# Kernel tuning notes

Hardware: AMD Instinct MI355X
Metric: run time of the kernel (lower is better)

Reference implementation:

```python
import jax, jax.numpy as jnp
import numpy as np

N_HEADS = 8   # n_heads
L = 2         # num_layers (= args.upper_T_num_layers)
H = 64        # hidden_size (= args.upper_T_hidden_dim)
F = 64        # input features
T = 12        # seq_len (= args.n_his)
N = 16384     # node_num (= LSTM batch dim)


def setup_inputs() -> dict:
    key = jax.random.key(0)
    ks = jax.random.split(key, 10)
    s = 0.05
    x = jax.random.normal(ks[0], (T, N, F), jnp.float32)
    # Stacked per-head, per-layer LSTM weights (PyTorch gate order: i, f, g, o).
    # Layer 0 input dim F == H so all layers stack cleanly.
    W_ih = jax.random.normal(ks[1], (L, N_HEADS, 4 * H, H), jnp.float32) * s
    W_hh = jax.random.normal(ks[2], (L, N_HEADS, 4 * H, H), jnp.float32) * s
    b_ih = jax.random.normal(ks[3], (L, N_HEADS, 4 * H), jnp.float32) * s
    b_hh = jax.random.normal(ks[4], (L, N_HEADS, 4 * H), jnp.float32) * s
    # Learned initial states (xavier-init nn.Parameters in the original).
    h0 = jax.random.normal(ks[5], (N_HEADS, L, N, H), jnp.float32) * s
    c0 = jax.random.normal(ks[6], (N_HEADS, L, N, H), jnp.float32) * s
    # 1x1 Conv2d(n_heads*n_his -> n_his): pure channel mixing.
    conv_w = jax.random.normal(ks[7], (T, N_HEADS * T), jnp.float32) * s
    conv_b = jax.random.normal(ks[8], (T,), jnp.float32) * s
    return {"x": x, "W_ih": W_ih, "W_hh": W_hh, "b_ih": b_ih, "b_hh": b_hh,
            "h0": h0, "c0": c0, "conv_w": conv_w, "conv_b": conv_b}


def _scan_lstm(gi, Whh, bhh, h0, c0):
    # gi: (T, heads, N, 4H) precomputed input contribution; h0/c0: (heads, N, H)
    def step(carry, g_t):
        h, c = carry
        gates = g_t + jnp.einsum('and,agd->ang', h, Whh) + bhh[:, None, :]
        i, f, g, o = jnp.split(gates, 4, axis=-1)
        c = jax.nn.sigmoid(f) * c + jax.nn.sigmoid(i) * jnp.tanh(g)
        h = jax.nn.sigmoid(o) * jnp.tanh(c)
        return (h, c), h
    (_, _), hs = jax.lax.scan(step, (h0, c0), gi)
    return hs  # (T, heads, N, H)


def reference(x, W_ih, W_hh, b_ih, b_hh, h0, c0, conv_w, conv_b):
    n_layers, n_heads = W_ih.shape[0], W_ih.shape[1]
    t_len, n_nodes, _ = x.shape
    hdim = W_hh.shape[-1]
    # Layer 0: input x is shared across heads; precompute input gates outside scan.
    gi = jnp.einsum('tnd,agd->tang', x, W_ih[0]) + b_ih[0][None, :, None, :]
    hs = _scan_lstm(gi, W_hh[0], b_hh[0], h0[:, 0], c0[:, 0])
    for l in range(1, n_layers):
        gi = jnp.einsum('tand,agd->tang', hs, W_ih[l]) + b_ih[l][None, :, None, :]
        hs = _scan_lstm(gi, W_hh[l], b_hh[l], h0[:, l], c0[:, l])
    # torch.cat over heads: head-major, then time -> channel dim = heads*T
    cat = jnp.transpose(hs, (1, 0, 2, 3)).reshape(n_heads * t_len, n_nodes, hdim)
    # 1x1 conv == channel mixing over (heads*T) -> T
    out = jnp.einsum('cnh,oc->onh', cat, conv_w) + conv_b[:, None, None]
    return out[None]  # (1, T, N, H)
```

## Files before the change

### kernel.cpp

```cpp
#include <hip/hip_runtime.h>
#include <hip/hip_bf16.h>


#define T_LEN 12
#define NHEADS 8
#define HD 64
#define NNODES 16384
#define MT 16
#define LDSP 72
#define WIH_ELEMS (2 * NHEADS * 4 * HD * HD)

typedef __bf16 bf16_t;
typedef __attribute__((ext_vector_type(2))) __bf16 bf16x2;
typedef __attribute__((ext_vector_type(4))) __bf16 bf16x4;
typedef __attribute__((ext_vector_type(8))) __bf16 bf16x8;
typedef __attribute__((ext_vector_type(4))) float f32x4;

#define MFMA16(a, b, c) __builtin_amdgcn_mfma_f32_16x16x32_bf16((a), (b), (c), 0, 0, 0)

#if __has_builtin(__builtin_amdgcn_exp2f)
#define EXP2(x) __builtin_amdgcn_exp2f(x)
#else
#define EXP2(x) exp2f(x)
#endif

__device__ __forceinline__ float fast_sigmoid(float v) {
    return __builtin_amdgcn_rcpf(1.0f + __expf(-v));
}
__device__ __forceinline__ float fast_tanh(float v) {
    return 2.0f * __builtin_amdgcn_rcpf(1.0f + __expf(-2.0f * v)) - 1.0f;
}

__device__ __forceinline__ bf16x8 load8f(const float* p) {
    f32x4 a = *(const f32x4*)p;
    f32x4 b = *(const f32x4*)(p + 4);
    bf16x8 r;
    r[0] = (bf16_t)a[0]; r[1] = (bf16_t)a[1]; r[2] = (bf16_t)a[2]; r[3] = (bf16_t)a[3];
    r[4] = (bf16_t)b[0]; r[5] = (bf16_t)b[1]; r[6] = (bf16_t)b[2]; r[7] = (bf16_t)b[3];
    return r;
}
__device__ __forceinline__ bf16x4 load4f(const float* p) {
    f32x4 a = *(const f32x4*)p;
    bf16x4 r;
    r[0] = (bf16_t)a[0]; r[1] = (bf16_t)a[1]; r[2] = (bf16_t)a[2]; r[3] = (bf16_t)a[3];
    return r;
}

template<bool SC>
__device__ __forceinline__ bf16x4 lstm_pointwise_sw(const f32x4* acc, float* creg) {
    float cn[4], so[4], tc[4];
    #pragma unroll
    for (int r = 0; r < 4; ++r) {
        float ei, ef, eg, eo;
        if (SC) {
            ei = EXP2(-acc[0][r]); ef = EXP2(-acc[1][r]);
            eg = EXP2(-acc[2][r]); eo = EXP2(-acc[3][r]);
        } else {
            ei = __expf(-acc[0][r]); ef = __expf(-acc[1][r]);
            eg = __expf(-2.0f * acc[2][r]); eo = __expf(-acc[3][r]);
        }
        float di = 1.0f + ei, df = 1.0f + ef, dg = 1.0f + eg, do_ = 1.0f + eo;
        float pif = di * df, pgo = dg * do_;
        float rr  = __builtin_amdgcn_rcpf(pif * pgo);
        float rif = rr * pgo, rgo = rr * pif;
        float sig_i  = rif * df;
        float sig_f  = rif * di;
        float tanh_g = 2.0f * (rgo * do_) - 1.0f;
        so[r] = rgo * dg;
        float cnr = sig_f * creg[r] + sig_i * tanh_g;
        cn[r] = cnr;
        creg[r] = cnr;
    }
    float d0 = 1.0f + EXP2(cn[0] * -2.885390082f);
    float d1 = 1.0f + EXP2(cn[1] * -2.885390082f);
    float d2 = 1.0f + EXP2(cn[2] * -2.885390082f);
    float d3 = 1.0f + EXP2(cn[3] * -2.885390082f);
    float p01 = d0 * d1, p23 = d2 * d3;
    float rr  = __builtin_amdgcn_rcpf(p01 * p23);
    float r01 = rr * p23, r23 = rr * p01;
    tc[0] = 2.0f * (r01 * d1) - 1.0f;
    tc[1] = 2.0f * (r01 * d0) - 1.0f;
    tc[2] = 2.0f * (r23 * d3) - 1.0f;
    tc[3] = 2.0f * (r23 * d2) - 1.0f;
    bf16x4 hv;
    hv[0] = (bf16_t)(so[0] * tc[0]);
    hv[1] = (bf16_t)(so[1] * tc[1]);
    hv[2] = (bf16_t)(so[2] * tc[2]);
    hv[3] = (bf16_t)(so[3] * tc[3]);
    return hv;
}

__global__ __launch_bounds__(256) void cvt_bf16_kernel(
    const float* __restrict__ src, bf16_t* __restrict__ dst, int n8)
{
    int i = blockIdx.x * 256 + threadIdx.x;
    if (i < n8) *(bf16x8*)(dst + (size_t)i * 8) = load8f(src + (size_t)i * 8);
}

__global__ __launch_bounds__(256) void cvt_w_kernel(
    const float* __restrict__ src, bf16_t* __restrict__ dst, int n8)
{
    int i = blockIdx.x * 256 + threadIdx.x;
    if (i >= n8) return;
    int row  = (i >> 3) & 255;
    int gate = row >> 6;
    float sc = (gate == 2) ? 2.885390082f : 1.442695041f;
    const float* p = src + (size_t)i * 8;
    f32x4 a = *(const f32x4*)p;
    f32x4 b = *(const f32x4*)(p + 4);
    bf16x8 r;
    r[0] = (bf16_t)(a[0]*sc); r[1] = (bf16_t)(a[1]*sc);
    r[2] = (bf16_t)(a[2]*sc); r[3] = (bf16_t)(a[3]*sc);
    r[4] = (bf16_t)(b[0]*sc); r[5] = (bf16_t)(b[1]*sc);
    r[6] = (bf16_t)(b[2]*sc); r[7] = (bf16_t)(b[3]*sc);
    *(bf16x8*)(dst + (size_t)i * 8) = r;
}

template<bool PREP>
__global__ __launch_bounds__(512, 4) void lstm_pipe_kernel(
    const float* __restrict__ xg,
    const bf16_t* __restrict__ xbf,
    const float* __restrict__ Wih,
    const float* __restrict__ Whh,
    const bf16_t* __restrict__ wbf,
    const float* __restrict__ bih,
    const float* __restrict__ bhh,
    const float* __restrict__ h0g,
    const float* __restrict__ c0g,
    bf16_t* __restrict__ hsw)
{
    __shared__ __align__(16) bf16_t xT[T_LEN][MT][LDSP];
    __shared__ __align__(16) bf16_t h0A[2][MT][LDSP];
    __shared__ __align__(16) bf16_t h1H[T_LEN + 1][MT][LDSP];
    __shared__ __align__(16) float  biasLds[2][4][4][16];

    const int tid  = threadIdx.x;
    const int w    = tid >> 6;
    const int lane = tid & 63;
    const int quad = lane >> 4;
    const int col  = lane & 15;
    const int lw   = w >> 2;
    const int wq   = w & 3;
    const int a    = blockIdx.x & (NHEADS - 1);
    const int nb   = (blockIdx.x >> 3) * MT;

    #pragma unroll
    for (int it = 0; it < 3; ++it) {
        int e    = (it * 512 + tid) * 8;
        int t    = e >> 10;
        int node = (e >> 6) & (MT - 1);
        int f    = e & (HD - 1);
        bf16x8 v;
        if (PREP) v = *(const bf16x8*)(xbf + ((size_t)t * NNODES + nb + node) * HD + f);
        else      v = load8f(xg + ((size_t)t * NNODES + nb + node) * HD + f);
        *(bf16x8*)&xT[t][node][f] = v;
    }
    {
        int e    = tid * 4;
        int l    = e >> 10;
        int node = (e >> 6) & (MT - 1);
        int hh   = e & (HD - 1);
        bf16x4 v = load4f(h0g + (((size_t)a * 2 + l) * NNODES + nb + node) * HD + hh);
        if (l == 0) *(bf16x4*)&h0A[0][node][hh] = v;
        else        *(bf16x4*)&h1H[0][node][hh] = v;
    }
    {
        int l   = tid >> 8;
        int r   = tid & 255;
        int wqi = r >> 6;
        int nii = (r >> 4) & 3;
        int gc  = r & 15;
        int off = (l * NHEADS + a) * 256 + nii * 64 + wqi * 16 + gc;
        float sc = PREP ? (nii == 2 ? 2.885390082f : 1.442695041f) : 1.0f;
        biasLds[l][wqi][nii][gc] = (bih[off] + bhh[off]) * sc;
    }

    bf16x8 wA[4][2], wB[4][2];
    #pragma unroll
    for (int ni = 0; ni < 4; ++ni)
        #pragma unroll
        for (int kf = 0; kf < 2; ++kf) {
            size_t off = (((size_t)lw * NHEADS + a) * 256 + (4 * ni + wq) * 16 + col) * HD
                       + kf * 32 + quad * 8;
            if (PREP) {
                wA[ni][kf] = *(const bf16x8*)(wbf + off);
                wB[ni][kf] = *(const bf16x8*)(wbf + WIH_ELEMS + off);
            } else {
                wA[ni][kf] = load8f(Wih + off);
                wB[ni][kf] = load8f(Whh + off);
            }
        }
    float creg[4];
    {
        f32x4 cv = *(const f32x4*)(c0g + (((size_t)a * 2 + lw) * NNODES + nb + col) * HD
                                   + wq * 16 + quad * 4);
        creg[0] = cv[0]; creg[1] = cv[1]; creg[2] = cv[2]; creg[3] = cv[3];
    }
    __syncthreads();

    int cur = 0;
    #pragma unroll 1
    for (int p = 0; p <= T_LEN; ++p) {
        const bool active = lw ? (p >= 1) : (p < T_LEN);
        if (active) {
            const bf16_t* P = lw ? &h0A[cur][0][0]     : &xT[p][0][0];
            const bf16_t* Q = lw ? &h1H[p - 1][0][0]   : &h0A[cur][0][0];
            bf16_t*       D = lw ? &h1H[p][0][0]       : &h0A[cur ^ 1][0][0];
            const int ro = col * LDSP + quad * 8;
            bf16x8 a0 = *(const bf16x8*)(P + ro);
            bf16x8 b0 = *(const bf16x8*)(Q + ro);
            f32x4 acc[4];
            #pragma unroll
            for (int ni = 0; ni < 4; ++ni) {
                f32x4 z = *(const f32x4*)&biasLds[lw][wq][ni][quad * 4];
                z = MFMA16(wA[ni][0], a0, z);
                acc[ni] = MFMA16(wB[ni][0], b0, z);
            }
            bf16x8 a1 = *(const bf16x8*)(P + ro + 32);
            bf16x8 b1 = *(const bf16x8*)(Q + ro + 32);
            #pragma unroll
            for (int ni = 0; ni < 4; ++ni) {
                f32x4 z = MFMA16(wA[ni][1], a1, acc[ni]);
                acc[ni] = MFMA16(wB[ni][1], b1, z);
            }
            bf16x4 hv = lstm_pointwise_sw<PREP>(acc, creg);
            *(bf16x4*)(D + col * LDSP + wq * 16 + quad * 4) = hv;
        }
        __syncthreads();
        cur ^= 1;
    }

    #pragma unroll
    for (int it = 0; it < 3; ++it) {
        int i    = it * 512 + tid;
        int t    = i >> 7;
        int c    = i & 127;
        int node = c >> 3;
        int h8   = (c & 7) * 8;
        *(bf16x8*)(hsw + ((size_t)(a * T_LEN + t) * NNODES + nb + node) * HD + h8) =
            *(const bf16x8*)&h1H[t + 1][node][h8];
    }
}

__global__ __launch_bounds__(256) void conv_reduce_kernel(
    const bf16_t* __restrict__ hsw,
    const float* __restrict__ cwg,
    const float* __restrict__ cbg,
    float* __restrict__ outg)
{
    int flat = blockIdx.x * 256 + threadIdx.x;
    int n  = flat >> 4;
    int h4 = (flat & 15) * 4;
    f32x4 acc[T_LEN];
    #pragma unroll
    for (int o = 0; o < T_LEN; ++o) {
        float b = cbg[o];
        acc[o][0] = b; acc[o][1] = b; acc[o][2] = b; acc[o][3] = b;
    }
    const bf16_t* src = hsw + (size_t)n * HD + h4;
    #pragma unroll 6
    for (int c = 0; c < NHEADS * T_LEN; ++c) {
        bf16x4 hv = *(const bf16x4*)(src + (size_t)c * NNODES * HD);
        float h0 = (float)hv[0], h1 = (float)hv[1], h2 = (float)hv[2], h3 = (float)hv[3];
        #pragma unroll
        for (int o = 0; o < T_LEN; ++o) {
            float cv = cwg[o * (NHEADS * T_LEN) + c];
            acc[o][0] += cv * h0; acc[o][1] += cv * h1;
            acc[o][2] += cv * h2; acc[o][3] += cv * h3;
        }
    }
    #pragma unroll
    for (int o = 0; o < T_LEN; ++o)
        *(f32x4*)(outg + ((size_t)o * NNODES + n) * HD + h4) = acc[o];
}

struct SmemT {
    __align__(16) bf16_t xT[T_LEN][MT][LDSP];
    __align__(16) bf16_t hA[2][2][MT][LDSP];
    __align__(16) float  cwf[T_LEN][NHEADS * T_LEN];
    __align__(16) float  cbf[T_LEN];
};

__global__ __launch_bounds__(256) void lstm_mono_kernel(
    const float* __restrict__ xg, const float* __restrict__ Wih,
    const float* __restrict__ Whh, const float* __restrict__ bih,
    const float* __restrict__ bhh, const float* __restrict__ h0g,
    const float* __restrict__ c0g, const float* __restrict__ cwg,
    const float* __restrict__ cbg, float* __restrict__ outg)
{
    __shared__ SmemT s;
    const int tid  = threadIdx.x;
    const int w    = tid >> 6;
    const int lane = tid & 63;
    const int quad = lane >> 4;
    const int col  = lane & 15;
    const int nb   = blockIdx.x * MT;

    #pragma unroll
    for (int it = 0; it < 6; ++it) {
        int ci   = it * 256 + tid;
        int e    = ci * 8;
        int t    = e >> 10;
        int node = (e >> 6) & (MT - 1);
        int f    = e & (HD - 1);
        *(bf16x8*)&s.xT[t][node][f] =
            load8f(xg + ((size_t)t * NNODES + nb + node) * HD + f);
    }
    for (int i = tid; i < T_LEN * NHEADS * T_LEN; i += 256)
        s.cwf[i / 96][i % 96] = cwg[i];
    if (tid < T_LEN) s.cbf[tid] = cbg[tid];

    float conv_acc[T_LEN][4];
    #pragma unroll
    for (int o = 0; o < T_LEN; ++o)
        #pragma unroll
        for (int r = 0; r < 4; ++r) conv_acc[o][r] = 0.0f;

    #pragma unroll 1
    for (int a = 0; a < NHEADS; ++a) {
        bf16x8 wih[2][4][2], whh[2][4][2];
        #pragma unroll
        for (int l = 0; l < 2; ++l)
            #pragma unroll
            for (int ni = 0; ni < 4; ++ni)
                #pragma unroll
                for (int kf = 0; kf < 2; ++kf) {
                    size_t off = (((size_t)l * NHEADS + a) * 256 + (4 * ni + w) * 16 + col) * HD
                               + kf * 32 + quad * 8;
                    wih[l][ni][kf] = load8f(Wih + off);
                    whh[l][ni][kf] = load8f(Whh + off);
                }
        float bias[2][4];
        #pragma unroll
        for (int l = 0; l < 2; ++l)
            #pragma unroll
            for (int ni = 0; ni < 4; ++ni) {
                int off = (l * NHEADS + a) * 256 + ni * 64 + w * 16 + col;
                bias[l][ni] = bih[off] + bhh[off];
            }
        float creg[2][4];
        #pragma unroll
        for (int l = 0; l < 2; ++l)
            #pragma unroll
            for (int r = 0; r < 4; ++r)
                creg[l][r] = c0g[(((size_t)a * 2 + l) * NNODES + nb + quad * 4 + r) * HD
                                 + w * 16 + col];
        {
            int e    = tid * 8;
            int l    = e >> 10;
            int node = (e >> 6) & (MT - 1);
            int hh   = e & (HD - 1);
            *(bf16x8*)&s.hA[l][0][node][hh] =
                load8f(h0g + (((size_t)a * 2 + l) * NNODES + nb + node) * HD + hh);
        }
        __syncthreads();

        int cur = 0;
        #pragma unroll 1
        for (int t = 0; t < T_LEN; ++t) {
            bf16x8 xa0 = *(const bf16x8*)&s.xT[t][col][quad * 8];
            bf16x8 xa1 = *(const bf16x8*)&s.xT[t][col][32 + quad * 8];
            bf16x8 ha0 = *(const bf16x8*)&s.hA[0][cur][col][quad * 8];
            bf16x8 ha1 = *(const bf16x8*)&s.hA[0][cur][col][32 + quad * 8];
            f32x4 acc[4];
            #pragma unroll
            for (int ni = 0; ni < 4; ++ni) {
                f32x4 z = {0.f, 0.f, 0.f, 0.f};
                z = MFMA16(xa0, wih[0][ni][0], z);
                z = MFMA16(xa1, wih[0][ni][1], z);
                z = MFMA16(ha0, whh[0][ni][0], z);
                z = MFMA16(ha1, whh[0][ni][1], z);
                acc[ni] = z;
            }
            #pragma unroll
            for (int r = 0; r < 4; ++r) {
                float ig = fast_sigmoid(acc[0][r] + bias[0][0]);
                float fg = fast_sigmoid(acc[1][r] + bias[0][1]);
                float gg = fast_tanh   (acc[2][r] + bias[0][2]);
                float og = fast_sigmoid(acc[3][r] + bias[0][3]);
                float cn = fg * creg[0][r] + ig * gg;
                creg[0][r] = cn;
                s.hA[0][cur ^ 1][quad * 4 + r][w * 16 + col] = (bf16_t)(og * fast_tanh(cn));
            }
            __syncthreads();
            bf16x8 pa0 = *(const bf16x8*)&s.hA[0][cur ^ 1][col][quad * 8];
            bf16x8 pa1 = *(const bf16x8*)&s.hA[0][cur ^ 1][col][32 + quad * 8];
            bf16x8 qa0 = *(const bf16x8*)&s.hA[1][cur][col][quad * 8];
            bf16x8 qa1 = *(const bf16x8*)&s.hA[1][cur][col][32 + quad * 8];
            #pragma unroll
            for (int ni = 0; ni < 4; ++ni) {
                f32x4 z = {0.f, 0.f, 0.f, 0.f};
                z = MFMA16(pa0, wih[1][ni][0], z);
                z = MFMA16(pa1, wih[1][ni][1], z);
                z = MFMA16(qa0, whh[1][ni][0], z);
                z = MFMA16(qa1, whh[1][ni][1], z);
                acc[ni] = z;
            }
            float hn[4];
            #pragma unroll
            for (int r = 0; r < 4; ++r) {
                float ig = fast_sigmoid(acc[0][r] + bias[1][0]);
                float fg = fast_sigmoid(acc[1][r] + bias[1][1]);
                float gg = fast_tanh   (acc[2][r] + bias[1][2]);
                float og = fast_sigmoid(acc[3][r] + bias[1][3]);
                float cn = fg * creg[1][r] + ig * gg;
                creg[1][r] = cn;
                hn[r] = og * fast_tanh(cn);
                s.hA[1][cur ^ 1][quad * 4 + r][w * 16 + col] = (bf16_t)hn[r];
            }
            #pragma unroll
            for (int o = 0; o < T_LEN; ++o) {
                float cv = s.cwf[o][a * T_LEN + t];
                #pragma unroll
                for (int r = 0; r < 4; ++r) conv_acc[o][r] += cv * hn[r];
            }
            __syncthreads();
            cur ^= 1;
        }
    }
    #pragma unroll
    for (int o = 0; o < T_LEN; ++o)
        #pragma unroll
        for (int r = 0; r < 4; ++r)
            outg[((size_t)o * NNODES + nb + quad * 4 + r) * HD + w * 16 + col] =
                conv_acc[o][r] + s.cbf[o];
}

extern "C" void kernel_launch(void* const* d_in, const int* in_sizes, int n_in,
                              void* d_out, int out_size, void* d_ws, size_t ws_size,
                              hipStream_t stream) {
    (void)in_sizes; (void)n_in; (void)out_size;
    const float* x   = (const float*)d_in[0];
    const float* Wih = (const float*)d_in[1];
    const float* Whh = (const float*)d_in[2];
    const float* bih = (const float*)d_in[3];
    const float* bhh = (const float*)d_in[4];
    const float* h0  = (const float*)d_in[5];
    const float* c0  = (const float*)d_in[6];
    const float* cw  = (const float*)d_in[7];
    const float* cb  = (const float*)d_in[8];
    const size_t hs_bytes = (size_t)NHEADS * T_LEN * NNODES * HD * sizeof(bf16_t);
    const size_t x_bytes  = (size_t)T_LEN * NNODES * HD * sizeof(bf16_t);
    const size_t w_bytes  = (size_t)2 * WIH_ELEMS * sizeof(bf16_t);
    if (ws_size >= hs_bytes + x_bytes + w_bytes) {
        bf16_t* hs  = (bf16_t*)d_ws;
        bf16_t* xbf = (bf16_t*)((char*)d_ws + hs_bytes);
        bf16_t* wbf = (bf16_t*)((char*)d_ws + hs_bytes + x_bytes);
        const int n8x = T_LEN * NNODES * HD / 8;
        const int n8w = WIH_ELEMS / 8;
        cvt_bf16_kernel<<<dim3(n8x / 256), dim3(256), 0, stream>>>(x, xbf, n8x);
        cvt_w_kernel<<<dim3((n8w + 255) / 256), dim3(256), 0, stream>>>(Wih, wbf, n8w);
        cvt_w_kernel<<<dim3((n8w + 255) / 256), dim3(256), 0, stream>>>(Whh, wbf + WIH_ELEMS, n8w);
        lstm_pipe_kernel<true><<<dim3((NNODES / MT) * NHEADS), dim3(512), 0, stream>>>(
            x, xbf, Wih, Whh, wbf, bih, bhh, h0, c0, hs);
        conv_reduce_kernel<<<dim3(NNODES * 16 / 256), dim3(256), 0, stream>>>(
            hs, cw, cb, (float*)d_out);
    } else if (ws_size >= hs_bytes) {
        bf16_t* hs = (bf16_t*)d_ws;
        lstm_pipe_kernel<false><<<dim3((NNODES / MT) * NHEADS), dim3(512), 0, stream>>>(
            x, nullptr, Wih, Whh, nullptr, bih, bhh, h0, c0, hs);
        conv_reduce_kernel<<<dim3(NNODES * 16 / 256), dim3(256), 0, stream>>>(
            hs, cw, cb, (float*)d_out);
    } else {
        lstm_mono_kernel<<<dim3(NNODES / MT), dim3(256), 0, stream>>>(
            x, Wih, Whh, bih, bhh, h0, c0, cw, cb, (float*)d_out);
    }
}
```

Before: 514.8 us.

## Store hidden states node-major, split per-layer wave paths, vectorise LSTM pointwise

The intermediate hidden-state buffer changes from channel-major (heads*T, N, H) to node-major (N, heads*T, H). The conv reduction therefore reads each node's channels contiguously instead of with a large stride, and the LSTM kernel writes them the same way. The per-timestep loop is split into separate layer-0 and layer-1 branches, with the next x fragment prefetched into registers and all LDS operand loads issued before the MFMA chains. The pointwise gate math is rewritten in vector form with one reciprocal per gate, dropping the shared-reciprocal trick, which adds rcp instructions in exchange for shorter dependency chains.

```diff
diff --git a/kernel.cpp b/kernel.cpp
--- a/kernel.cpp
+++ b/kernel.cpp
@@ -8,6 +8,7 @@
 #define NNODES 16384
 #define MT 16
 #define LDSP 72
+#define NCH (NHEADS * T_LEN)
 #define WIH_ELEMS (2 * NHEADS * 4 * HD * HD)
 
 typedef __bf16 bf16_t;
@@ -46,47 +47,37 @@
     return r;
 }
 
+__device__ __forceinline__ f32x4 exp2n4(f32x4 v) {
+    f32x4 r;
+    #pragma unroll
+    for (int i = 0; i < 4; ++i) r[i] = EXP2(-v[i]);
+    return r;
+}
+__device__ __forceinline__ f32x4 rcp4(f32x4 v) {
+    f32x4 r;
+    #pragma unroll
+    for (int i = 0; i < 4; ++i) r[i] = __builtin_amdgcn_rcpf(v[i]);
+    return r;
+}
+
 template<bool SC>
-__device__ __forceinline__ bf16x4 lstm_pointwise_sw(const f32x4* acc, float* creg) {
-    float cn[4], so[4], tc[4];
-    #pragma unroll
-    for (int r = 0; r < 4; ++r) {
-        float ei, ef, eg, eo;
-        if (SC) {
-            ei = EXP2(-acc[0][r]); ef = EXP2(-acc[1][r]);
-            eg = EXP2(-acc[2][r]); eo = EXP2(-acc[3][r]);
-        } else {
-            ei = __expf(-acc[0][r]); ef = __expf(-acc[1][r]);
-            eg = __expf(-2.0f * acc[2][r]); eo = __expf(-acc[3][r]);
-        }
-        float di = 1.0f + ei, df = 1.0f + ef, dg = 1.0f + eg, do_ = 1.0f + eo;
-        float pif = di * df, pgo = dg * do_;
-        float rr  = __builtin_amdgcn_rcpf(pif * pgo);
-        float rif = rr * pgo, rgo = rr * pif;
-        float sig_i  = rif * df;
-        float sig_f  = rif * di;
-        float tanh_g = 2.0f * (rgo * do_) - 1.0f;
-        so[r] = rgo * dg;
-        float cnr = sig_f * creg[r] + sig_i * tanh_g;
-        cn[r] = cnr;
-        creg[r] = cnr;
-    }
-    float d0 = 1.0f + EXP2(cn[0] * -2.885390082f);
-    float d1 = 1.0f + EXP2(cn[1] * -2.885390082f);
-    float d2 = 1.0f + EXP2(cn[2] * -2.885390082f);
-    float d3 = 1.0f + EXP2(cn[3] * -2.885390082f);
-    float p01 = d0 * d1, p23 = d2 * d3;
-    float rr  = __builtin_amdgcn_rcpf(p01 * p23);
-    float r01 = rr * p23, r23 = rr * p01;
-    tc[0] = 2.0f * (r01 * d1) - 1.0f;
-    tc[1] = 2.0f * (r01 * d0) - 1.0f;
-    tc[2] = 2.0f * (r23 * d3) - 1.0f;
-    tc[3] = 2.0f * (r23 * d2) - 1.0f;
+__device__ __forceinline__ bf16x4 lstm_pointwise_v(const f32x4* acc, f32x4& creg) {
+    f32x4 gi = acc[0], gf = acc[1], gg = acc[2], go = acc[3];
+    if (!SC) {
+        gi = gi * 1.442695041f; gf = gf * 1.442695041f;
+        gg = gg * 2.885390082f; go = go * 1.442695041f;
+    }
+    f32x4 si = rcp4(exp2n4(gi) + 1.0f);
+    f32x4 sf = rcp4(exp2n4(gf) + 1.0f);
+    f32x4 tg = 2.0f * rcp4(exp2n4(gg) + 1.0f) - 1.0f;
+    f32x4 so = rcp4(exp2n4(go) + 1.0f);
+    f32x4 cn = sf * creg + si * tg;
+    creg = cn;
+    f32x4 tc = 2.0f * rcp4(exp2n4(cn * 2.885390082f) + 1.0f) - 1.0f;
+    f32x4 h  = so * tc;
     bf16x4 hv;
-    hv[0] = (bf16_t)(so[0] * tc[0]);
-    hv[1] = (bf16_t)(so[1] * tc[1]);
-    hv[2] = (bf16_t)(so[2] * tc[2]);
-    hv[3] = (bf16_t)(so[3] * tc[3]);
+    hv[0] = (bf16_t)h[0]; hv[1] = (bf16_t)h[1];
+    hv[2] = (bf16_t)h[2]; hv[3] = (bf16_t)h[3];
     return hv;
 }
 
@@ -190,55 +181,76 @@
                 wB[ni][kf] = load8f(Whh + off);
             }
         }
-    float creg[4];
-    {
-        f32x4 cv = *(const f32x4*)(c0g + (((size_t)a * 2 + lw) * NNODES + nb + col) * HD
-                                   + wq * 16 + quad * 4);
-        creg[0] = cv[0]; creg[1] = cv[1]; creg[2] = cv[2]; creg[3] = cv[3];
-    }
+    f32x4 creg = *(const f32x4*)(c0g + (((size_t)a * 2 + lw) * NNODES + nb + col) * HD
+                                 + wq * 16 + quad * 4);
     __syncthreads();
+
+    const int ro = col * LDSP + quad * 8;
+    bf16x8 px0, px1;
+    if (lw == 0) {
+        px0 = *(const bf16x8*)&xT[0][col][quad * 8];
+        px1 = *(const bf16x8*)&xT[0][col][32 + quad * 8];
+    }
 
     int cur = 0;
     #pragma unroll 1
     for (int p = 0; p <= T_LEN; ++p) {
-        const bool active = lw ? (p >= 1) : (p < T_LEN);
-        if (active) {
-            const bf16_t* P = lw ? &h0A[cur][0][0]     : &xT[p][0][0];
-            const bf16_t* Q = lw ? &h1H[p - 1][0][0]   : &h0A[cur][0][0];
-            bf16_t*       D = lw ? &h1H[p][0][0]       : &h0A[cur ^ 1][0][0];
-            const int ro = col * LDSP + quad * 8;
-            bf16x8 a0 = *(const bf16x8*)(P + ro);
-            bf16x8 b0 = *(const bf16x8*)(Q + ro);
-            f32x4 acc[4];
-            #pragma unroll
-            for (int ni = 0; ni < 4; ++ni) {
-                f32x4 z = *(const f32x4*)&biasLds[lw][wq][ni][quad * 4];
-                z = MFMA16(wA[ni][0], a0, z);
-                acc[ni] = MFMA16(wB[ni][0], b0, z);
-            }
-            bf16x8 a1 = *(const bf16x8*)(P + ro + 32);
-            bf16x8 b1 = *(const bf16x8*)(Q + ro + 32);
-            #pragma unroll
-            for (int ni = 0; ni < 4; ++ni) {
-                f32x4 z = MFMA16(wA[ni][1], a1, acc[ni]);
-                acc[ni] = MFMA16(wB[ni][1], b1, z);
-            }
-            bf16x4 hv = lstm_pointwise_sw<PREP>(acc, creg);
-            *(bf16x4*)(D + col * LDSP + wq * 16 + quad * 4) = hv;
+        if (lw == 0) {
+            if (p < T_LEN) {
+                bf16x8 h0f = *(const bf16x8*)(&h0A[cur][0][0] + ro);
+                bf16x8 h1f = *(const bf16x8*)(&h0A[cur][0][0] + ro + 32);
+                f32x4 acc[4];
+                #pragma unroll
+                for (int ni = 0; ni < 4; ++ni) {
+                    f32x4 z = *(const f32x4*)&biasLds[0][wq][ni][quad * 4];
+                    z = MFMA16(wA[ni][0], px0, z);
+                    z = MFMA16(wA[ni][1], px1, z);
+                    z = MFMA16(wB[ni][0], h0f, z);
+                    acc[ni] = MFMA16(wB[ni][1], h1f, z);
+                }
+                if (p + 1 < T_LEN) {
+                    px0 = *(const bf16x8*)&xT[p + 1][col][quad * 8];
+                    px1 = *(const bf16x8*)&xT[p + 1][col][32 + quad * 8];
+                }
+                bf16x4 hv = lstm_pointwise_v<PREP>(acc, creg);
+                *(bf16x4*)(&h0A[cur ^ 1][0][0] + col * LDSP + wq * 16 + quad * 4) = hv;
+            }
+        } else {
+            if (p >= 1) {
+                const bf16_t* P = &h0A[cur][0][0];
+                const bf16_t* Q = &h1H[p - 1][0][0];
+                bf16x8 p0f = *(const bf16x8*)(P + ro);
+                bf16x8 p1f = *(const bf16x8*)(P + ro + 32);
+                bf16x8 q0f = *(const bf16x8*)(Q + ro);
+                bf16x8 q1f = *(const bf16x8*)(Q + ro + 32);
+                f32x4 acc[4];
+                #pragma unroll
+                for (int ni = 0; ni < 4; ++ni) {
+                    f32x4 z = *(const f32x4*)&biasLds[1][wq][ni][quad * 4];
+                    z = MFMA16(wA[ni][0], p0f, z);
+                    z = MFMA16(wA[ni][1], p1f, z);
+                    z = MFMA16(wB[ni][0], q0f, z);
+                    acc[ni] = MFMA16(wB[ni][1], q1f, z);
+                }
+                bf16x4 hv = lstm_pointwise_v<PREP>(acc, creg);
+                *(bf16x4*)(&h1H[p][0][0] + col * LDSP + wq * 16 + quad * 4) = hv;
+            }
         }
         __syncthreads();
         cur ^= 1;
     }
 
-    #pragma unroll
-    for (int it = 0; it < 3; ++it) {
-        int i    = it * 512 + tid;
-        int t    = i >> 7;
-        int c    = i & 127;
-        int node = c >> 3;
-        int h8   = (c & 7) * 8;
-        *(bf16x8*)(hsw + ((size_t)(a * T_LEN + t) * NNODES + nb + node) * HD + h8) =
-            *(const bf16x8*)&h1H[t + 1][node][h8];
+    {
+        int node = tid >> 5;
+        int sub  = tid & 31;
+        #pragma unroll
+        for (int k = 0; k < 3; ++k) {
+            int c8 = k * 32 + sub;
+            int t  = c8 >> 3;
+            int h8 = (c8 & 7) * 8;
+            *(bf16x8*)(hsw + ((size_t)(nb + node) * NCH + a * T_LEN + t) * HD + h8) =
+                *(const bf16x8*)&h1H[t + 1][node][h8];
+        }
     }
 }
 
@@ -257,14 +269,14 @@
         float b = cbg[o];
         acc[o][0] = b; acc[o][1] = b; acc[o][2] = b; acc[o][3] = b;
     }
-    const bf16_t* src = hsw + (size_t)n * HD + h4;
-    #pragma unroll 6
-    for (int c = 0; c < NHEADS * T_LEN; ++c) {
-        bf16x4 hv = *(const bf16x4*)(src + (size_t)c * NNODES * HD);
+    const bf16_t* src = hsw + (size_t)n * (NCH * HD) + h4;
+    #pragma unroll 8
+    for (int c = 0; c < NCH; ++c) {
+        bf16x4 hv = *(const bf16x4*)(src + (size_t)c * HD);
         float h0 = (float)hv[0], h1 = (float)hv[1], h2 = (float)hv[2], h3 = (float)hv[3];
         #pragma unroll
         for (int o = 0; o < T_LEN; ++o) {
-            float cv = cwg[o * (NHEADS * T_LEN) + c];
+            float cv = cwg[o * NCH + c];
             acc[o][0] += cv * h0; acc[o][1] += cv * h1;
             acc[o][2] += cv * h2; acc[o][3] += cv * h3;
         }
@@ -277,7 +289,7 @@
 struct SmemT {
     __align__(16) bf16_t xT[T_LEN][MT][LDSP];
     __align__(16) bf16_t hA[2][2][MT][LDSP];
-    __align__(16) float  cwf[T_LEN][NHEADS * T_LEN];
+    __align__(16) float  cwf[T_LEN][NCH];
     __align__(16) float  cbf[T_LEN];
 };
 
@@ -306,7 +318,7 @@
         *(bf16x8*)&s.xT[t][node][f] =
             load8f(xg + ((size_t)t * NNODES + nb + node) * HD + f);
     }
-    for (int i = tid; i < T_LEN * NHEADS * T_LEN; i += 256)
+    for (int i = tid; i < T_LEN * NCH; i += 256)
         s.cwf[i / 96][i % 96] = cwg[i];
     if (tid < T_LEN) s.cbf[tid] = cbg[tid];
 
@@ -439,7 +451,7 @@
     const float* c0  = (const float*)d_in[6];
     const float* cw  = (const float*)d_in[7];
     const float* cb  = (const float*)d_in[8];
-    const size_t hs_bytes = (size_t)NHEADS * T_LEN * NNODES * HD * sizeof(bf16_t);
+    const size_t hs_bytes = (size_t)NCH * NNODES * HD * sizeof(bf16_t);
     const size_t x_bytes  = (size_t)T_LEN * NNODES * HD * sizeof(bf16_t);
     const size_t w_bytes  = (size_t)2 * WIH_ELEMS * sizeof(bf16_t);
     if (ws_size >= hs_bytes + x_bytes + w_bytes) {
```

New measurement: 492.3 us. 1.05x faster.
